# Optimization experiments

Measured on AMD Instinct MI355X. Metric: run time of the kernel, lower is better.

## Reference

```python
import jax, jax.numpy as jnp
import numpy as np

B = 32
NODES = [200000, 1024, 256, 32]
CH = [1, 32, 64, 128]
EDGES = [2048000, 262144, 8192]
NCLS = 10


def _wn(V, g):
    # PyTorch weight_norm (dim=0): each output row rescaled to norm g[o]
    return g[:, None] * V / jnp.linalg.norm(V, axis=1, keepdims=True)


def _fgl(x, src, dst, n_out, W, b):
    # x: (B, C_in, N_in); sparse random-adjacency downsample then channel mix
    xt = jnp.moveaxis(x, 2, 0)                                   # (N_in, B, C_in)
    gathered = xt[src]                                           # (E, B, C_in)
    pooled = jax.ops.segment_sum(gathered, dst, num_segments=n_out)  # (N_out, B, C_in)
    return jnp.einsum('nbc,oc->bon', pooled, W) + b[None, :, None]   # (B, C_out, N_out)


def setup_inputs() -> dict:
    key = jax.random.key(0)
    ks = jax.random.split(key, 20)
    d = {}
    d['x'] = jax.random.normal(ks[0], (B, NODES[0]), jnp.float32)
    for i in range(3):
        e = EDGES[i]
        n_in, n_out = NODES[i], NODES[i + 1]
        d[f'edge_src{i}'] = jax.random.randint(ks[1 + 2 * i], (e,), 0, n_in, jnp.int32)
        d[f'edge_dst{i}'] = jnp.sort(jax.random.randint(ks[2 + 2 * i], (e,), 0, n_out, jnp.int32))
    for i in range(3):
        cin, cout = CH[i], CH[i + 1]
        d[f'V{i}'] = jax.random.normal(ks[7 + 3 * i], (cout, cin), jnp.float32) * 0.1
        d[f'g{i}'] = jnp.ones((cout,), jnp.float32)
        d[f'b{i}'] = jnp.zeros((cout,), jnp.float32)
    d['Vfc'] = jax.random.normal(ks[16], (NCLS, CH[-1] * NODES[-1]), jnp.float32) * 0.02
    d['gfc'] = jnp.ones((NCLS,), jnp.float32)
    d['bfc'] = jnp.zeros((NCLS,), jnp.float32)
    return d


def reference(x, edge_src0, edge_dst0, edge_src1, edge_dst1, edge_src2, edge_dst2,
              V0, g0, b0, V1, g1, b1, V2, g2, b2, Vfc, gfc, bfc):
    z = x[:, None, :]                                            # (B, 1, N_in)
    z = _fgl(z, edge_src0, edge_dst0, NODES[1], _wn(V0, g0), b0)  # (B, 32, 1024)
    z = _fgl(z, edge_src1, edge_dst1, NODES[2], _wn(V1, g1), b1)  # (B, 64, 256)
    z = _fgl(z, edge_src2, edge_dst2, NODES[3], _wn(V2, g2), b2)  # (B, 128, 32)
    flat = z.reshape(z.shape[0], -1)                             # (B, 4096)
    return flat @ _wn(Vfc, gfc).T + bfc                          # (B, NCLS)
```

## Files before the change

kernel.cpp:

```cpp
#include <hip/hip_runtime.h>
#include <math.h>

#define N0 200000
#define N1 1024
#define N2 256
#define N3 32
#define NE0 2048000
#define NE1 262144
#define NE2 8192
#define BATCH 32
#define NCLS 10
#define NB 4
#define SRC_PER_B 50000
#define TBLOCKS 1563
#define PREBLOCKS (N1 + TBLOCKS)

typedef _Float16 h2 __attribute__((ext_vector_type(2)));
typedef _Float16 h8 __attribute__((ext_vector_type(8)));

__device__ __forceinline__ int lower_bound_i(const int* __restrict__ a, int n, int key) {
    int lo = 0, hi = n;
    while (lo < hi) {
        int mid = (lo + hi) >> 1;
        if (a[mid] < key) lo = mid + 1; else hi = mid;
    }
    return lo;
}

__global__ __launch_bounds__(256) void k_pre(const float* __restrict__ x,
                                             h2* __restrict__ xt,
                                             const int* __restrict__ src,
                                             const int* __restrict__ dst,
                                             int* __restrict__ esrc,
                                             int* __restrict__ bstart) {
    const int i = blockIdx.x;
    const int tid = threadIdx.x;
    if (i >= N1) {
        const int t = i - N1;
        __shared__ float tile[32][129];
        const int col0 = t * 128;
        #pragma unroll
        for (int pass = 0; pass < 4; ++pass) {
            int row = (tid >> 5) + 8 * pass;
            int j4 = (tid & 31) * 4;
            int col = col0 + j4;
            if (col < N0) {
                const float4 v = *reinterpret_cast<const float4*>(&x[row * N0 + col]);
                tile[row][j4]     = v.x;
                tile[row][j4 + 1] = v.y;
                tile[row][j4 + 2] = v.z;
                tile[row][j4 + 3] = v.w;
            }
        }
        __syncthreads();
        h8* xt8 = reinterpret_cast<h8*>(xt);
        #pragma unroll
        for (int k = 0; k < 2; ++k) {
            int cl = (tid >> 2) + 64 * k;
            int col = col0 + cl;
            int c4 = tid & 3;
            if (col < N0) {
                h8 v;
                #pragma unroll
                for (int ii = 0; ii < 8; ++ii)
                    v[ii] = (_Float16)tile[8 * c4 + ii][cl];
                xt8[col * 4 + c4] = v;
            }
        }
        return;
    }
    const int n = i;
    const int e0 = lower_bound_i(dst, NE0, n);
    const int e1 = lower_bound_i(dst, NE0, n + 1);
    const int len = e1 - e0;
    const int wave = tid >> 6, lane = tid & 63;
    const int q0 = e0 + (len * wave) / 4;
    const int q1 = e0 + (len * (wave + 1)) / 4;
    __shared__ int wcnt[4][NB];
    __shared__ int wbase[4][NB];

    int c0 = 0, c1 = 0, c2 = 0, c3 = 0;
    for (int base = q0; base < q1; base += 64) {
        int e = base + lane;
        int b = -1;
        if (e < q1) b = src[e] / SRC_PER_B;
        c0 += __popcll(__ballot(b == 0));
        c1 += __popcll(__ballot(b == 1));
        c2 += __popcll(__ballot(b == 2));
        c3 += __popcll(__ballot(b == 3));
    }
    if (lane == 0) { wcnt[wave][0] = c0; wcnt[wave][1] = c1; wcnt[wave][2] = c2; wcnt[wave][3] = c3; }
    __syncthreads();
    if (tid == 0) {
        int acc = e0;
        #pragma unroll
        for (int b = 0; b < NB; ++b) {
            bstart[n * (NB + 1) + b] = acc;
            #pragma unroll
            for (int w = 0; w < 4; ++w) { wbase[w][b] = acc; acc += wcnt[w][b]; }
        }
        bstart[n * (NB + 1) + NB] = acc;
    }
    __syncthreads();

    int u0 = wbase[wave][0], u1 = wbase[wave][1], u2 = wbase[wave][2], u3 = wbase[wave][3];
    for (int base = q0; base < q1; base += 64) {
        int e = base + lane;
        int s = 0, b = -1;
        if (e < q1) { s = src[e]; b = s / SRC_PER_B; }
        unsigned long long m0 = __ballot(b == 0);
        unsigned long long m1 = __ballot(b == 1);
        unsigned long long m2 = __ballot(b == 2);
        unsigned long long m3 = __ballot(b == 3);
        unsigned long long lt = (1ull << lane) - 1ull;
        if (b == 0)      esrc[u0 + __popcll(m0 & lt)] = s;
        else if (b == 1) esrc[u1 + __popcll(m1 & lt)] = s;
        else if (b == 2) esrc[u2 + __popcll(m2 & lt)] = s;
        else if (b == 3) esrc[u3 + __popcll(m3 & lt)] = s;
        u0 += __popcll(m0); u1 += __popcll(m1); u2 += __popcll(m2); u3 += __popcll(m3);
    }
}

__global__ __launch_bounds__(128) void k_gather0s(const h8* __restrict__ table,
                                                  const int* __restrict__ esrc,
                                                  const int* __restrict__ bstart,
                                                  _Float16* __restrict__ p0p) {
    const int b = blockIdx.x & (NB - 1);
    const int n = blockIdx.x >> 2;
    const int q0 = bstart[n * (NB + 1) + b];
    const int q1 = bstart[n * (NB + 1) + b + 1];
    const int tid = threadIdx.x;
    const int b4 = tid & 3;
    const int g  = tid >> 2;
    float acc[8] = {0.f, 0.f, 0.f, 0.f, 0.f, 0.f, 0.f, 0.f};
    int e = q0 + g;
    for (; e + 96 < q1; e += 128) {
        int s0 = esrc[e];
        int s1 = esrc[e + 32];
        int s2 = esrc[e + 64];
        int s3 = esrc[e + 96];
        h8 v0 = table[s0 * 4 + b4];
        h8 v1 = table[s1 * 4 + b4];
        h8 v2 = table[s2 * 4 + b4];
        h8 v3 = table[s3 * 4 + b4];
        #pragma unroll
        for (int i = 0; i < 8; ++i)
            acc[i] += (float)v0[i] + (float)v1[i] + (float)v2[i] + (float)v3[i];
    }
    for (; e < q1; e += 32) {
        int s = esrc[e];
        h8 v = table[s * 4 + b4];
        #pragma unroll
        for (int i = 0; i < 8; ++i) acc[i] += (float)v[i];
    }
    __shared__ float red[32][33];
    #pragma unroll
    for (int i = 0; i < 8; ++i) red[g][b4 * 8 + i] = acc[i];
    __syncthreads();
    #pragma unroll
    for (int s = 16; s >= 1; s >>= 1) {
        if (g < s) {
            #pragma unroll
            for (int i = 0; i < 8; ++i)
                red[g][b4 * 8 + i] += red[g + s][b4 * 8 + i];
        }
        __syncthreads();
    }
    if (tid < 32) p0p[(b * N1 + n) * 32 + tid] = (_Float16)red[0][tid];
}

__global__ __launch_bounds__(256) void k_gather1w(
    const h8* __restrict__ p0p, const int* __restrict__ src,
    const int* __restrict__ dst, _Float16* __restrict__ out_h,
    float* __restrict__ cnt_out,
    const float* __restrict__ V0, const float* __restrict__ g0, const float* __restrict__ b0,
    const float* __restrict__ V1, const float* __restrict__ g1, const float* __restrict__ b1,
    const float* __restrict__ V2, const float* __restrict__ g2, const float* __restrict__ b2,
    const float* __restrict__ Vfc, const float* __restrict__ gfc,
    float* __restrict__ M_, float* __restrict__ Q2_, float* __restrict__ R2_,
    float* __restrict__ B4_) {
    const int tid = threadIdx.x;
    if (blockIdx.x < N2) {
        const int n = blockIdx.x;
        const int e0 = lower_bound_i(dst, NE1, n);
        const int e1 = lower_bound_i(dst, NE1, n + 1);
        const int b4 = tid & 3;
        const int g  = tid >> 2;
        float acc[8] = {0.f, 0.f, 0.f, 0.f, 0.f, 0.f, 0.f, 0.f};
        for (int e = e0 + g; e < e1; e += 64) {
            int s = src[e];
            h8 v0 = p0p[0 * N1 * 4 + s * 4 + b4];
            h8 v1 = p0p[1 * N1 * 4 + s * 4 + b4];
            h8 v2 = p0p[2 * N1 * 4 + s * 4 + b4];
            h8 v3 = p0p[3 * N1 * 4 + s * 4 + b4];
            #pragma unroll
            for (int i = 0; i < 8; ++i)
                acc[i] += ((float)v0[i] + (float)v1[i]) + ((float)v2[i] + (float)v3[i]);
        }
        __shared__ float red[64][33];
        #pragma unroll
        for (int i = 0; i < 8; ++i) red[g][b4 * 8 + i] = acc[i];
        __syncthreads();
        #pragma unroll
        for (int s = 32; s >= 1; s >>= 1) {
            if (g < s) {
                #pragma unroll
                for (int i = 0; i < 8; ++i)
                    red[g][b4 * 8 + i] += red[g + s][b4 * 8 + i];
            }
            __syncthreads();
        }
        if (tid < 32) out_h[n * 32 + tid] = (_Float16)red[0][tid];
        else if (tid == 32) cnt_out[n] = (float)(e1 - e0);
        return;
    }
    const int k = blockIdx.x - N2;
    __shared__ float w0[32], u[64], v[64], p[128], q[128], r[128];
    __shared__ float redA[8][32], redB[8][32], redC[8][32], redD[8][32];
    __shared__ float nnred[4];
    __shared__ float scale_s;

    if (tid < 32) {
        float val = V0[tid];
        w0[tid] = g0[tid] * val / fabsf(val);
    }
    __syncthreads();
    if (tid < 64) {
        float nn = 0.f;
        #pragma unroll
        for (int c = 0; c < 32; ++c) { float t = V1[tid * 32 + c]; nn += t * t; }
        float inv = g1[tid] * rsqrtf(nn);
        float su = 0.f, sv = 0.f;
        #pragma unroll
        for (int c = 0; c < 32; ++c) {
            float w = V1[tid * 32 + c] * inv;
            su += w * w0[c]; sv += w * b0[c];
        }
        u[tid] = su; v[tid] = sv;
    }
    __syncthreads();
    if (tid < 128) {
        float nn = 0.f;
        #pragma unroll
        for (int c = 0; c < 64; ++c) { float t = V2[tid * 64 + c]; nn += t * t; }
        float inv = g2[tid] * rsqrtf(nn);
        float sp = 0.f, sq = 0.f, sr = 0.f;
        #pragma unroll
        for (int c = 0; c < 64; ++c) {
            float w = V2[tid * 64 + c] * inv;
            sp += w * u[c]; sq += w * v[c]; sr += w * b1[c];
        }
        p[tid] = sp; q[tid] = sq; r[tid] = sr;
    }
    __syncthreads();

    const int n3 = tid & 31, og = tid >> 5;
    float nn = 0.f, mk = 0.f, mq = 0.f, mr = 0.f, mb = 0.f;
    #pragma unroll
    for (int i = 0; i < 16; ++i) {
        int o = og + 8 * i;
        float w = Vfc[k * 4096 + tid + 256 * i];
        nn += w * w;
        mk += w * p[o]; mq += w * q[o]; mr += w * r[o]; mb += w * b2[o];
    }
    #pragma unroll
    for (int off = 32; off; off >>= 1) nn += __shfl_xor(nn, off);
    if ((tid & 63) == 0) nnred[tid >> 6] = nn;
    redA[og][n3] = mk; redB[og][n3] = mq; redC[og][n3] = mr; redD[og][n3] = mb;
    __syncthreads();
    if (tid == 0) {
        float s = nnred[0] + nnred[1] + nnred[2] + nnred[3];
        scale_s = gfc[k] * rsqrtf(s);
    }
    __syncthreads();
    if (tid < 32) {
        float smk = 0.f, smq = 0.f, smr = 0.f, smb = 0.f;
        #pragma unroll
        for (int i = 0; i < 8; ++i) {
            smk += redA[i][tid]; smq += redB[i][tid];
            smr += redC[i][tid]; smb += redD[i][tid];
        }
        float scale = scale_s;
        M_[k * 32 + tid]  = scale * smk;
        Q2_[k * 32 + tid] = scale * smq;
        R2_[k * 32 + tid] = scale * smr;
        float bs = scale * smb;
        #pragma unroll
        for (int off = 16; off; off >>= 1) bs += __shfl_xor(bs, off);
        if (tid == 0) B4_[k] = bs;
    }
}

__global__ __launch_bounds__(256) void k_gather2(const h8* __restrict__ table,
                                                 const int* __restrict__ src,
                                                 const int* __restrict__ dst,
                                                 const float* __restrict__ cnt_in,
                                                 float* __restrict__ out_f,
                                                 float* __restrict__ cnt_out,
                                                 float* __restrict__ t_out) {
    const int n = blockIdx.x;
    const int e0 = lower_bound_i(dst, NE2, n);
    const int e1 = lower_bound_i(dst, NE2, n + 1);
    const int tid = threadIdx.x;
    const int b4 = tid & 3;
    const int g  = tid >> 2;
    float acc[8] = {0.f, 0.f, 0.f, 0.f, 0.f, 0.f, 0.f, 0.f};
    float tacc = 0.f;
    for (int e = e0 + g; e < e1; e += 64) {
        int s = src[e];
        h8 v = table[s * 4 + b4];
        #pragma unroll
        for (int i = 0; i < 8; ++i) acc[i] += (float)v[i];
        if (b4 == 0) tacc += cnt_in[s];
    }
    __shared__ float red[64][33];
    __shared__ float tred[64];
    #pragma unroll
    for (int i = 0; i < 8; ++i) red[g][b4 * 8 + i] = acc[i];
    if (b4 == 0) tred[g] = tacc;
    __syncthreads();
    #pragma unroll
    for (int s = 32; s >= 1; s >>= 1) {
        if (g < s) {
            #pragma unroll
            for (int i = 0; i < 8; ++i)
                red[g][b4 * 8 + i] += red[g + s][b4 * 8 + i];
            if (b4 == 0) tred[g] += tred[g + s];
        }
        __syncthreads();
    }
    if (tid < 32) out_f[n * 32 + tid] = red[0][tid];
    else if (tid == 32) cnt_out[n] = (float)(e1 - e0);
    else if (tid == 33) t_out[n] = tred[0];
}

__global__ __launch_bounds__(64) void k_final(const float* __restrict__ M_,
                                              const float* __restrict__ Q2_,
                                              const float* __restrict__ R2_,
                                              const float* __restrict__ B4_,
                                              const float* __restrict__ bfc,
                                              const float* __restrict__ S2,
                                              const float* __restrict__ T2,
                                              const float* __restrict__ cnt2,
                                              float* __restrict__ out) {
    const int k = blockIdx.x;
    const int tid = threadIdx.x;
    __shared__ float Kc_s;
    float kc = 0.f;
    if (tid < 32)
        kc = Q2_[k * 32 + tid] * T2[tid] + R2_[k * 32 + tid] * cnt2[tid];
    #pragma unroll
    for (int off = 16; off; off >>= 1) kc += __shfl_xor(kc, off);
    if (tid == 0) Kc_s = kc + B4_[k] + bfc[k];
    __syncthreads();
    if (tid < 32) {
        int b = tid;
        float s = 0.f;
        #pragma unroll
        for (int n = 0; n < 32; ++n) s += M_[k * 32 + n] * S2[n * 32 + b];
        out[b * NCLS + k] = s + Kc_s;
    }
}

extern "C" void kernel_launch(void* const* d_in, const int* in_sizes, int n_in,
                              void* d_out, int out_size, void* d_ws, size_t ws_size,
                              hipStream_t stream) {
    const float* x   = (const float*)d_in[0];
    const int* src0  = (const int*)d_in[1];
    const int* dst0  = (const int*)d_in[2];
    const int* src1  = (const int*)d_in[3];
    const int* dst1  = (const int*)d_in[4];
    const int* src2  = (const int*)d_in[5];
    const int* dst2  = (const int*)d_in[6];
    const float* V0  = (const float*)d_in[7];
    const float* g0  = (const float*)d_in[8];
    const float* b0  = (const float*)d_in[9];
    const float* V1  = (const float*)d_in[10];
    const float* g1  = (const float*)d_in[11];
    const float* b1  = (const float*)d_in[12];
    const float* V2  = (const float*)d_in[13];
    const float* g2  = (const float*)d_in[14];
    const float* b2  = (const float*)d_in[15];
    const float* Vfc = (const float*)d_in[16];
    const float* gfc = (const float*)d_in[17];
    const float* bfc = (const float*)d_in[18];

    char* ws = (char*)d_ws;
    _Float16* xt   = (_Float16*)(ws);
    int* esrc      = (int*)(ws + 12800000);
    int* bstart    = (int*)(ws + 20992000);
    _Float16* P0p  = (_Float16*)(ws + 21012480);
    _Float16* S1h  = (_Float16*)(ws + 21274624);
    float* cnt1    = (float*)(ws + 21291008);
    float* S2      = (float*)(ws + 21292032);
    float* T2      = (float*)(ws + 21296128);
    float* cnt2    = (float*)(ws + 21296256);
    float* M_      = (float*)(ws + 21296384);
    float* Q2_     = (float*)(ws + 21297664);
    float* R2_     = (float*)(ws + 21298944);
    float* B4_     = (float*)(ws + 21300224);

    k_pre<<<PREBLOCKS, 256, 0, stream>>>(x, (h2*)xt, src0, dst0, esrc, bstart);
    k_gather0s<<<N1 * NB, 128, 0, stream>>>((const h8*)xt, esrc, bstart,
                                            (_Float16*)P0p);
    k_gather1w<<<N2 + NCLS, 256, 0, stream>>>((const h8*)P0p, src1, dst1,
                                              S1h, cnt1,
                                              V0, g0, b0, V1, g1, b1,
                                              V2, g2, b2, Vfc, gfc,
                                              M_, Q2_, R2_, B4_);
    k_gather2<<<N3, 256, 0, stream>>>((const h8*)S1h, src2, dst2, cnt1,
                                      S2, cnt2, T2);
    k_final<<<NCLS, 64, 0, stream>>>(M_, Q2_, R2_, B4_, bfc, S2, T2, cnt2,
                                     (float*)d_out);
}
```

Measured before the change: 70.39 us.

## Compact edge source indices to 16-bit and find segment bounds via windowed scan

Edge sources are stored as 16-bit offsets relative to each batch bucket, which halves the bytes written by k_pre and read by the gather kernel. The gather adds the bucket base back and reads the indices with nontemporal loads. Segment boundaries are now found by scanning a window around the expected position (mean segment length 2000) instead of two global binary searches, with a binary-search fallback when the boundary is not in the window. The window scan reads more dst entries per block and relies on the destinations being roughly uniform.

```diff
diff --git a/kernel.cpp b/kernel.cpp
--- a/kernel.cpp
+++ b/kernel.cpp
@@ -12,6 +12,8 @@
 #define NCLS 10
 #define NB 4
 #define SRC_PER_B 50000
+#define SEG_LEN 2000
+#define WPAD 3072
 #define TBLOCKS 1563
 #define PREBLOCKS (N1 + TBLOCKS)
 
@@ -31,7 +33,7 @@
                                              h2* __restrict__ xt,
                                              const int* __restrict__ src,
                                              const int* __restrict__ dst,
-                                             int* __restrict__ esrc,
+                                             unsigned short* __restrict__ esrc,
                                              int* __restrict__ bstart) {
     const int i = blockIdx.x;
     const int tid = threadIdx.x;
@@ -70,8 +72,32 @@
         return;
     }
     const int n = i;
-    const int e0 = lower_bound_i(dst, NE0, n);
-    const int e1 = lower_bound_i(dst, NE0, n + 1);
+    __shared__ int sE0, sE1;
+    if (tid == 0) { sE0 = -1; sE1 = -1; }
+    __syncthreads();
+    {
+        int W0 = n * SEG_LEN - WPAD; if (W0 < 0) W0 = 0;
+        int W1 = (n + 1) * SEG_LEN + WPAD; if (W1 > NE0) W1 = NE0;
+        for (int e = W0 + tid; e < W1; e += 256) {
+            int cur = dst[e];
+            int prev = (e == 0) ? -1 : dst[e - 1];
+            if (prev < n && cur >= n) sE0 = e;
+            if (prev < n + 1 && cur >= n + 1) sE1 = e;
+        }
+        __syncthreads();
+        if (tid == 0) {
+            int t0 = sE0, t1 = sE1;
+            if (t0 < 0) t0 = lower_bound_i(dst, NE0, n);
+            if (t1 < 0) {
+                if (sE0 >= 0 && W1 == NE0) t1 = NE0;
+                else t1 = lower_bound_i(dst, NE0, n + 1);
+            }
+            sE0 = t0; sE1 = t1;
+        }
+        __syncthreads();
+    }
+    const int e0 = sE0;
+    const int e1 = sE1;
     const int len = e1 - e0;
     const int wave = tid >> 6, lane = tid & 63;
     const int q0 = e0 + (len * wave) / 4;
@@ -113,16 +139,16 @@
         unsigned long long m2 = __ballot(b == 2);
         unsigned long long m3 = __ballot(b == 3);
         unsigned long long lt = (1ull << lane) - 1ull;
-        if (b == 0)      esrc[u0 + __popcll(m0 & lt)] = s;
-        else if (b == 1) esrc[u1 + __popcll(m1 & lt)] = s;
-        else if (b == 2) esrc[u2 + __popcll(m2 & lt)] = s;
-        else if (b == 3) esrc[u3 + __popcll(m3 & lt)] = s;
+        if (b == 0)      esrc[u0 + __popcll(m0 & lt)] = (unsigned short)s;
+        else if (b == 1) esrc[u1 + __popcll(m1 & lt)] = (unsigned short)(s - SRC_PER_B);
+        else if (b == 2) esrc[u2 + __popcll(m2 & lt)] = (unsigned short)(s - 2 * SRC_PER_B);
+        else if (b == 3) esrc[u3 + __popcll(m3 & lt)] = (unsigned short)(s - 3 * SRC_PER_B);
         u0 += __popcll(m0); u1 += __popcll(m1); u2 += __popcll(m2); u3 += __popcll(m3);
     }
 }
 
 __global__ __launch_bounds__(128) void k_gather0s(const h8* __restrict__ table,
-                                                  const int* __restrict__ esrc,
+                                                  const unsigned short* __restrict__ esrc,
                                                   const int* __restrict__ bstart,
                                                   _Float16* __restrict__ p0p) {
     const int b = blockIdx.x & (NB - 1);
@@ -132,13 +158,14 @@
     const int tid = threadIdx.x;
     const int b4 = tid & 3;
     const int g  = tid >> 2;
+    const int sbase = b * SRC_PER_B;
     float acc[8] = {0.f, 0.f, 0.f, 0.f, 0.f, 0.f, 0.f, 0.f};
     int e = q0 + g;
     for (; e + 96 < q1; e += 128) {
-        int s0 = esrc[e];
-        int s1 = esrc[e + 32];
-        int s2 = esrc[e + 64];
-        int s3 = esrc[e + 96];
+        int s0 = sbase + (int)__builtin_nontemporal_load(esrc + e);
+        int s1 = sbase + (int)__builtin_nontemporal_load(esrc + e + 32);
+        int s2 = sbase + (int)__builtin_nontemporal_load(esrc + e + 64);
+        int s3 = sbase + (int)__builtin_nontemporal_load(esrc + e + 96);
         h8 v0 = table[s0 * 4 + b4];
         h8 v1 = table[s1 * 4 + b4];
         h8 v2 = table[s2 * 4 + b4];
@@ -148,7 +175,7 @@
             acc[i] += (float)v0[i] + (float)v1[i] + (float)v2[i] + (float)v3[i];
     }
     for (; e < q1; e += 32) {
-        int s = esrc[e];
+        int s = sbase + (int)__builtin_nontemporal_load(esrc + e);
         h8 v = table[s * 4 + b4];
         #pragma unroll
         for (int i = 0; i < 8; ++i) acc[i] += (float)v[i];
@@ -386,19 +413,19 @@
     const float* bfc = (const float*)d_in[18];
 
     char* ws = (char*)d_ws;
-    _Float16* xt   = (_Float16*)(ws);
-    int* esrc      = (int*)(ws + 12800000);
-    int* bstart    = (int*)(ws + 20992000);
-    _Float16* P0p  = (_Float16*)(ws + 21012480);
-    _Float16* S1h  = (_Float16*)(ws + 21274624);
-    float* cnt1    = (float*)(ws + 21291008);
-    float* S2      = (float*)(ws + 21292032);
-    float* T2      = (float*)(ws + 21296128);
-    float* cnt2    = (float*)(ws + 21296256);
-    float* M_      = (float*)(ws + 21296384);
-    float* Q2_     = (float*)(ws + 21297664);
-    float* R2_     = (float*)(ws + 21298944);
-    float* B4_     = (float*)(ws + 21300224);
+    _Float16* xt          = (_Float16*)(ws);
+    unsigned short* esrc  = (unsigned short*)(ws + 12800000);
+    int* bstart           = (int*)(ws + 16896000);
+    _Float16* P0p         = (_Float16*)(ws + 16916480);
+    _Float16* S1h         = (_Float16*)(ws + 17178624);
+    float* cnt1           = (float*)(ws + 17195008);
+    float* S2             = (float*)(ws + 17196032);
+    float* T2             = (float*)(ws + 17200128);
+    float* cnt2           = (float*)(ws + 17200256);
+    float* M_             = (float*)(ws + 17200384);
+    float* Q2_            = (float*)(ws + 17201664);
+    float* R2_            = (float*)(ws + 17202944);
+    float* B4_            = (float*)(ws + 17204224);
 
     k_pre<<<PREBLOCKS, 256, 0, stream>>>(x, (h2*)xt, src0, dst0, esrc, bstart);
     k_gather0s<<<N1 * NB, 128, 0, stream>>>((const h8*)xt, esrc, bstart,
```

After: 77.17 us. +9.6%, slower.
